# Performance work log

Measured on AMD Instinct MI355X. Metric: run time of the kernel, lower is better.

Reference implementation:

```python
import jax, jax.numpy as jnp
from jax import lax
import numpy as np

B, C, H, W, D = 4, 128, 32, 32, 32
NH = 4                 # num_heads (4*NH == 16 fc input channels)
DH = C // NH           # head dim = 32
N = H * W * D          # input_size = 32768
PROJ = 64              # proj_size
EPS = 1e-12


def setup_inputs() -> dict:
    key = jax.random.key(0)
    ks = jax.random.split(key, 12)
    s = 0.02
    return {
        "x": jax.random.normal(ks[0], (B, C, H, W, D), jnp.float32),
        "Wqkvv": jax.random.normal(ks[1], (4 * C, C), jnp.float32) * s,   # qkv_bias=False
        "W_fc": jax.random.normal(ks[2], (16, 4 * NH), jnp.float32) * s,  # Conv2d 1x1
        "b_fc": jnp.zeros((16,), jnp.float32),
        "W_dep": jax.random.normal(ks[3], (C, 16, 3, 3, 3), jnp.float32) * 0.05,  # groups=DH -> in/grp=16
        "b_dep": jnp.zeros((C,), jnp.float32),
        "W_E": jax.random.normal(ks[4], (PROJ, N), jnp.float32) * s,  # E = F (shared weights)
        "b_E": jnp.zeros((PROJ,), jnp.float32),
        "temperature": jnp.ones((NH, 1, 1), jnp.float32),
        "temperature2": jnp.ones((NH, 1, 1), jnp.float32),
        "rate": jnp.full((1,), 0.5, jnp.float32),
        "rate2": jnp.full((1,), 0.5, jnp.float32),
        "W_out": jax.random.normal(ks[5], (C // 2, C), jnp.float32) * s,
        "b_out": jnp.zeros((C // 2,), jnp.float32),
        "W_out2": jax.random.normal(ks[6], (C // 2, C), jnp.float32) * s,
        "b_out2": jnp.zeros((C // 2,), jnp.float32),
    }


def _l2norm(t):
    return t / jnp.maximum(jnp.linalg.norm(t, axis=-1, keepdims=True), EPS)


def reference(x, Wqkvv, W_fc, b_fc, W_dep, b_dep, W_E, b_E,
              temperature, temperature2, rate, rate2,
              W_out, b_out, W_out2, b_out2):
    Bc, Cc, Hc, Wc, Dc = x.shape
    Nc = Hc * Wc * Dc
    # tokens: [B, N, C]
    xf = jnp.transpose(x, (0, 2, 3, 4, 1)).reshape(Bc, Nc, Cc)
    qkvv = xf @ Wqkvv.T  # [B, N, 4C]

    # ---- fused grouped-conv branch ----
    f_all = jnp.transpose(qkvv.reshape(Bc, Nc, 4 * NH, DH), (0, 2, 1, 3))  # [B,16,N,DH]
    f = jnp.einsum('oi,bind->bond', W_fc, f_all) + b_fc[None, :, None, None]  # 1x1 conv
    f_conv = jnp.transpose(f, (0, 3, 1, 2)).reshape(Bc, 16 * DH, Hc, Wc, Dc)
    out_conv = lax.conv_general_dilated(
        f_conv, W_dep, window_strides=(1, 1, 1), padding='SAME',
        dimension_numbers=('NCDHW', 'OIDHW', 'NCDHW'), feature_group_count=DH)
    out_conv = out_conv + b_dep[None, :, None, None, None]
    out_conv = jnp.transpose(out_conv, (0, 2, 3, 4, 1)).reshape(Bc, Nc, Cc)

    # ---- dual attention ----
    qkvv5 = jnp.transpose(qkvv.reshape(Bc, Nc, 4, NH, DH), (2, 0, 3, 1, 4))  # [4,B,nh,N,dh]
    q = jnp.swapaxes(qkvv5[0], -2, -1)    # [B,nh,dh,N]
    k = jnp.swapaxes(qkvv5[1], -2, -1)
    v_CA = jnp.swapaxes(qkvv5[2], -2, -1)
    v_SA = jnp.swapaxes(qkvv5[3], -2, -1)

    k_proj = k @ W_E.T + b_E              # [B,nh,dh,proj]  (E)
    v_SA_proj = v_SA @ W_E.T + b_E        # shared weights   (F)

    qn = _l2norm(q)
    kn = _l2norm(k)

    # channel attention: [B,nh,dh,dh]
    attn_CA = jax.nn.softmax(jnp.einsum('bhdn,bhen->bhde', qn, kn) * temperature, axis=-1)
    x_CA = jnp.transpose(attn_CA @ v_CA, (0, 3, 1, 2)).reshape(Bc, Nc, Cc)  # [B,N,C]

    # spatial (Linformer-style) attention: [B,nh,N,proj]
    attn_SA = jax.nn.softmax(
        jnp.einsum('bhdn,bhdp->bhnp', qn, k_proj) * temperature2, axis=-1)
    x_SA = jnp.einsum('bhnp,bhdp->bhnd', attn_SA, v_SA_proj)  # [B,nh,N,dh]
    x_SA = jnp.transpose(x_SA, (0, 3, 1, 2)).reshape(Bc, Nc, Cc)  # faithful to torch permute

    x_SA = x_SA @ W_out.T + b_out    # [B,N,C/2]
    x_CA = x_CA @ W_out2.T + b_out2  # [B,N,C/2]
    x_attn = jnp.concatenate([x_SA, x_CA], axis=-1)
    return rate * x_attn + rate2 * out_conv
```

## Files before the change

### kernel.cpp

```cpp
#include <hip/hip_runtime.h>
#include <hip/hip_bf16.h>

typedef unsigned short u16;
typedef __attribute__((ext_vector_type(8))) short bf16x8;
typedef __attribute__((ext_vector_type(4))) float f32x4;

#define MFMA16(a,b,c) __builtin_amdgcn_mfma_f32_16x16x32_bf16((a),(b),(c),0,0,0)

__device__ __forceinline__ float bf2f(u16 u){ union{unsigned int i; float f;} v; v.i=((unsigned int)u)<<16; return v.f; }
__device__ __forceinline__ u16 f2bf(float f){ union{float f; unsigned int i;} v; v.f=f; unsigned int r=v.i+0x7fffu+((v.i>>16)&1u); return (u16)(r>>16); }
__device__ __forceinline__ unsigned int pk2(float a, float b){
  __hip_bfloat162 h = __float22bfloat162_rn(make_float2(a,b));
  union{ __hip_bfloat162 h; unsigned int u; } v; v.h = h; return v.u;
}

__global__ __launch_bounds__(256) void kcvt3(const float* __restrict__ WE, u16* __restrict__ WEb,
                                             const float* __restrict__ Wq, u16* __restrict__ Wqb,
                                             const float* __restrict__ Wo, u16* __restrict__ Wob){
  int bid = blockIdx.x;
  const float* src; u16* dst; int base;
  if(bid < 2048){ src = WE; dst = WEb; base = bid*1024; }
  else if(bid < 2112){ src = Wq; dst = Wqb; base = (bid-2048)*1024; }
  else { src = Wo; dst = Wob; base = (bid-2112)*1024; }
  int i = base + threadIdx.x*4;
  float4 v = *(const float4*)(src + i);
  ushort4 o; o.x = f2bf(v.x); o.y = f2bf(v.y); o.z = f2bf(v.z); o.w = f2bf(v.w);
  *(ushort4*)(dst + i) = o;
}

#define K1PAD 136
__global__ __launch_bounds__(256) void k1_qkvv(const float* __restrict__ x, const u16* __restrict__ Wqb, u16* __restrict__ qkvvT){
  __shared__ u16 lB[128*K1PAD];
  const int tile = blockIdx.x;
  const int b  = tile >> 8;
  const int n0 = (tile & 255) << 7;
  const int tid = threadIdx.x;
  const float* xb = x + (size_t)b*128*32768;
  {
    const int cb = (tid >> 4) << 1;
    const int m  = tid & 15;
    const int t8 = m << 3;
    const int swz = (m & 3) << 3;
    unsigned int* basep = (unsigned int*)lB;
    #pragma unroll
    for(int r=0;r<4;++r){
      const int c = cb + (r<<5);
      const float4* p0 = (const float4*)(xb + (size_t)c*32768 + n0 + t8);
      const float4* p1 = (const float4*)(xb + (size_t)(c+1)*32768 + n0 + t8);
      float4 a0 = p0[0], a1 = p0[1];
      float4 b0 = p1[0], b1 = p1[1];
      const int rot = (swz + c) & 127;
      int di = t8*68 + (rot>>1);
      basep[di      ] = pk2(a0.x, b0.x);
      basep[di+  68 ] = pk2(a0.y, b0.y);
      basep[di+ 136 ] = pk2(a0.z, b0.z);
      basep[di+ 204 ] = pk2(a0.w, b0.w);
      basep[di+ 272 ] = pk2(a1.x, b1.x);
      basep[di+ 340 ] = pk2(a1.y, b1.y);
      basep[di+ 408 ] = pk2(a1.z, b1.z);
      basep[di+ 476 ] = pk2(a1.w, b1.w);
    }
  }
  __syncthreads();
  const int wave = tid >> 6, lane = tid & 63;
  const int wm = (wave & 1) << 6;
  const int wn = (wave >> 1) << 6;
  const int lm = lane & 15, lq = lane >> 4;
  u16* outb = qkvvT + (size_t)b*512*32768;
  for(int s=0;s<4;++s){
    const int oc0 = s << 7;
    f32x4 acc[4][4] = {};
    const u16* Arow = Wqb + (oc0 + wm + lm)*128 + lq*8;
    #pragma unroll
    for(int ks=0; ks<4; ++ks){
      bf16x8 af[4], bfr[4];
      #pragma unroll
      for(int mt=0;mt<4;++mt) af[mt] = *(const bf16x8*)(Arow + mt*2048 + ks*32);
      #pragma unroll
      for(int nt=0;nt<4;++nt){
        const int tr = wn + nt*16 + lm;
        const int rot = ((((tr>>3)&3)<<3) + ks*32 + lq*8) & 127;
        bfr[nt] = *(const bf16x8*)(&lB[tr*K1PAD + rot]);
      }
      #pragma unroll
      for(int mt=0;mt<4;++mt)
        #pragma unroll
        for(int nt=0;nt<4;++nt)
          acc[mt][nt] = MFMA16(af[mt], bfr[nt], acc[mt][nt]);
    }
    #pragma unroll
    for(int mt=0;mt<4;++mt){
      const int ocr = oc0 + wm + mt*16 + lq*4;
      #pragma unroll
      for(int nt=0;nt<4;++nt){
        const int n = n0 + wn + nt*16 + lm;
        #pragma unroll
        for(int r=0;r<4;++r) outb[(size_t)(ocr+r)*32768 + n] = f2bf(acc[mt][nt][r]);
      }
    }
  }
}

__global__ void k2_weff(const float* __restrict__ Wdep, const float* __restrict__ Wfc,
                        const float* __restrict__ bdep, const float* __restrict__ bfc,
                        float* __restrict__ W_eff, float* __restrict__ bias_eff){
  int idx = blockIdx.x*256 + threadIdx.x;
  if(idx < 55296){
    int ol = idx & 3;
    int k  = (idx >> 2) % 27;
    int j  = (idx / 108) & 15;
    int g  = idx / 1728;
    int oc = g*4 + ol;
    float s = 0.f;
    for(int o=0;o<16;++o) s += Wdep[(oc*16 + o)*27 + k] * Wfc[o*16 + j];
    W_eff[idx] = s;
  }
  if(idx < 128){
    float s = bdep[idx];
    for(int o=0;o<16;++o){
      float wsum = 0.f;
      for(int k=0;k<27;++k) wsum += Wdep[(idx*16 + o)*27 + k];
      s += wsum * bfc[o];
    }
    bias_eff[idx] = s;
  }
}

__global__ __launch_bounds__(256) void k2b_norms(const u16* __restrict__ qkvvT, float* __restrict__ invn){
  const int b = blockIdx.x >> 8, c = blockIdx.x & 255;
  const u16* row = qkvvT + ((size_t)b*512 + c)*32768;
  float s = 0.f;
  for(int n = threadIdx.x*8; n < 32768; n += 2048){
    bf16x8 v = *(const bf16x8*)(row + n);
    #pragma unroll
    for(int j=0;j<8;++j){ float f = bf2f((u16)v[j]); s += f*f; }
  }
  for(int off=32; off; off>>=1) s += __shfl_down(s, off, 64);
  __shared__ float wsum[4];
  if((threadIdx.x & 63)==0) wsum[threadIdx.x>>6] = s;
  __syncthreads();
  if(threadIdx.x==0){
    float t = wsum[0]+wsum[1]+wsum[2]+wsum[3];
    invn[blockIdx.x] = 1.0f / fmaxf(sqrtf(t), 1e-12f);
  }
}

__global__ __launch_bounds__(256) void k3_proj(const u16* __restrict__ qkvvT, const u16* __restrict__ WEb,
                                               float* __restrict__ kp, float* __restrict__ vp){
  const int kc = blockIdx.x;
  const int b  = blockIdx.y;
  const int ts = blockIdx.z >> 1;
  const int rh = (blockIdx.z & 1) << 6;
  const int wave = threadIdx.x >> 6, lane = threadIdx.x & 63;
  const int lm = lane & 15, lq = lane >> 4;
  const int coff = ts ? 384 : 128;
  const u16* Arow = qkvvT + ((size_t)b*512 + coff + rh + wave*16 + lm)*32768 + kc*1024 + lq*8;
  f32x4 acc[4] = {};
  for(int ks=0; ks<32; ++ks){
    bf16x8 af = *(const bf16x8*)(Arow + ks*32);
    #pragma unroll
    for(int nt=0;nt<4;++nt){
      bf16x8 bfr = *(const bf16x8*)(WEb + (size_t)(nt*16 + lm)*32768 + kc*1024 + ks*32 + lq*8);
      acc[nt] = MFMA16(af, bfr, acc[nt]);
    }
  }
  float* out = (ts ? vp : kp) + (size_t)b*128*64;
  const int r0 = rh + wave*16 + lq*4;
  #pragma unroll
  for(int nt=0;nt<4;++nt){
    const int p = nt*16 + lm;
    #pragma unroll
    for(int r=0;r<4;++r) atomicAdd(&out[(r0+r)*64 + p], acc[nt][r]);
  }
}

__global__ __launch_bounds__(64) void k4_gram(const u16* __restrict__ qkvvT, float* __restrict__ G){
  const int kc = blockIdx.x, b = blockIdx.y, h = blockIdx.z;
  const int lane = threadIdx.x, lm = lane & 15, lq = lane >> 4;
  const u16* qb = qkvvT + ((size_t)b*512 + h*32)*32768 + kc*512 + lq*8;
  const u16* kb = qb + (size_t)128*32768;
  f32x4 acc[2][2] = {};
  for(int ks=0; ks<16; ++ks){
    bf16x8 af[2], bfr[2];
    af[0]  = *(const bf16x8*)(qb + (size_t)lm*32768 + ks*32);
    af[1]  = *(const bf16x8*)(qb + (size_t)(16+lm)*32768 + ks*32);
    bfr[0] = *(const bf16x8*)(kb + (size_t)lm*32768 + ks*32);
    bfr[1] = *(const bf16x8*)(kb + (size_t)(16+lm)*32768 + ks*32);
    #pragma unroll
    for(int mt=0;mt<2;++mt)
      #pragma unroll
      for(int nt=0;nt<2;++nt) acc[mt][nt] = MFMA16(af[mt], bfr[nt], acc[mt][nt]);
  }
  float* Gb = G + (size_t)(b*4 + h)*1024;
  #pragma unroll
  for(int mt=0;mt<2;++mt)
    #pragma unroll
    for(int nt=0;nt<2;++nt)
      #pragma unroll
      for(int r=0;r<4;++r){
        int d = mt*16 + lq*4 + r, e = nt*16 + lm;
        atomicAdd(&Gb[d*32 + e], acc[mt][nt][r]);
      }
}

__global__ __launch_bounds__(256) void k4b_softmax_m2(const float* __restrict__ G, const float* __restrict__ invn,
                                                      const float* __restrict__ temp, const float* __restrict__ Wout2,
                                                      u16* __restrict__ M2){
  const int b = blockIdx.x >> 2, h = blockIdx.x & 3;
  __shared__ float A[32][33];
  const float* Gb = G + (size_t)(b*4 + h)*1024;
  const float* inb = invn + b*256;
  const float th = temp[h];
  const int tid = threadIdx.x;
  if(tid < 32){
    const int d = tid;
    const float iq = inb[h*32 + d];
    float row[32]; float mx = -1e30f;
    #pragma unroll
    for(int e=0;e<32;++e){
      float v = Gb[d*32+e] * iq * inb[128 + h*32 + e] * th;
      row[e] = v; mx = fmaxf(mx, v);
    }
    float s = 0.f;
    #pragma unroll
    for(int e=0;e<32;++e){ float ee = __expf(row[e]-mx); row[e] = ee; s += ee; }
    const float rs = 1.0f/s;
    #pragma unroll
    for(int e=0;e<32;++e) A[d][e] = row[e]*rs;
  }
  __syncthreads();
  for(int o = tid; o < 2048; o += 256){
    const int j = o >> 5, e = o & 31;
    float s = 0.f;
    #pragma unroll
    for(int d=0;d<32;++d) s += Wout2[j*128 + h*32 + d] * A[d][e];
    M2[((size_t)b*64 + j)*128 + h*32 + e] = f2bf(s);
  }
}

__global__ __launch_bounds__(256) void k5_xsa(const u16* __restrict__ qkvvT, const float* __restrict__ kp,
                                              const float* __restrict__ vp, const float* __restrict__ invn,
                                              const float* __restrict__ bE, const float* __restrict__ temp2,
                                              u16* __restrict__ xsa){
  __shared__ __align__(16) u16 L[14336];
  __shared__ float liqt[32];
  u16* lkAh = L;
  u16* lkAl = L + 2560;
  u16* lvAh = L + 5120;
  u16* lvAl = L + 7424;
  u16* Pl   = L + 9728;
  const int b = blockIdx.z, h = blockIdx.y;
  const int tid = threadIdx.x;
  const float t2 = temp2[h];
  {
    const int p = tid >> 2, d8 = (tid & 3) << 3;
    const float be = bE[p];
    const float* kpb = kp + ((size_t)b*128 + h*32)*64;
    #pragma unroll
    for(int j=0;j<8;++j){
      float v = kpb[(size_t)(d8+j)*64 + p] + be;
      u16 hi = f2bf(v);
      lkAh[p*40 + d8 + j] = hi;
      lkAl[p*40 + d8 + j] = f2bf(v - bf2f(hi));
    }
  }
  {
    const int d = tid >> 3, p8 = (tid & 7) << 3;
    const float* vpb = vp + ((size_t)b*128 + h*32)*64;
    #pragma unroll
    for(int j=0;j<8;++j){
      float v = vpb[(size_t)d*64 + p8 + j] + bE[p8+j];
      u16 hi = f2bf(v);
      lvAh[d*72 + p8 + j] = hi;
      lvAl[d*72 + p8 + j] = f2bf(v - bf2f(hi));
    }
  }
  if(tid < 32) liqt[tid] = invn[b*256 + h*32 + tid] * t2;
  __syncthreads();
  const int wave = tid >> 6, lane = tid & 63;
  const int lm = lane & 15, lq = lane >> 4;
  const int tokw = blockIdx.x*256 + wave*64;
  const u16* qb = qkvvT + ((size_t)b*512 + h*32)*32768;
  float iq[8];
  #pragma unroll
  for(int j=0;j<8;++j) iq[j] = liqt[lq*8+j];
  u16* PW = Pl + wave*1152 + lm*72;
  u16* ob = xsa + (((size_t)b*4 + h)*32)*32768;
  for(int nt=0; nt<4; ++nt){
    const int tok = tokw + nt*16 + lm;
    union { u16 u[8]; bf16x8 v; } qh, ql;
    #pragma unroll
    for(int j=0;j<8;++j){
      float qv = bf2f(qb[(size_t)(lq*8+j)*32768 + tok]) * iq[j];
      u16 hi = f2bf(qv);
      qh.u[j] = hi;
      ql.u[j] = f2bf(qv - bf2f(hi));
    }
    f32x4 accS[4];
    #pragma unroll
    for(int mt=0;mt<4;++mt){
      bf16x8 Ah = *(const bf16x8*)(lkAh + (mt*16+lm)*40 + lq*8);
      bf16x8 Al = *(const bf16x8*)(lkAl + (mt*16+lm)*40 + lq*8);
      f32x4 a = {};
      a = MFMA16(Ah, qh.v, a);
      a = MFMA16(Ah, ql.v, a);
      a = MFMA16(Al, qh.v, a);
      accS[mt] = a;
    }
    float mx = -1e30f;
    #pragma unroll
    for(int mt=0;mt<4;++mt)
      mx = fmaxf(mx, fmaxf(fmaxf(accS[mt][0],accS[mt][1]), fmaxf(accS[mt][2],accS[mt][3])));
    mx = fmaxf(mx, __shfl_xor(mx,16));
    mx = fmaxf(mx, __shfl_xor(mx,32));
    float pexp[4][4];
    float sum = 0.f;
    #pragma unroll
    for(int mt=0;mt<4;++mt)
      #pragma unroll
      for(int r=0;r<4;++r){ float e = __expf(accS[mt][r]-mx); pexp[mt][r]=e; sum+=e; }
    sum += __shfl_xor(sum,16);
    sum += __shfl_xor(sum,32);
    const float rinv = 1.0f/sum;
    #pragma unroll
    for(int mt=0;mt<4;++mt){
      *(unsigned int*)(PW + mt*16 + lq*4)     = pk2(pexp[mt][0], pexp[mt][1]);
      *(unsigned int*)(PW + mt*16 + lq*4 + 2) = pk2(pexp[mt][2], pexp[mt][3]);
    }
    f32x4 accO[2] = {};
    #pragma unroll
    for(int ks=0;ks<2;++ks){
      bf16x8 Pb = *(const bf16x8*)(PW + ks*32 + lq*8);
      #pragma unroll
      for(int mt=0;mt<2;++mt){
        bf16x8 Avh = *(const bf16x8*)(lvAh + (mt*16+lm)*72 + ks*32 + lq*8);
        bf16x8 Avl = *(const bf16x8*)(lvAl + (mt*16+lm)*72 + ks*32 + lq*8);
        accO[mt] = MFMA16(Avh, Pb, accO[mt]);
        accO[mt] = MFMA16(Avl, Pb, accO[mt]);
      }
    }
    #pragma unroll
    for(int mt=0;mt<2;++mt)
      #pragma unroll
      for(int r=0;r<4;++r)
        ob[(size_t)(mt*16+lq*4+r)*32768 + tok] = f2bf(accO[mt][r]*rinv);
  }
}

#define CSX 36
#define CSZ 360
__global__ __launch_bounds__(256,6) void kconv(const u16* __restrict__ qkvvT, const float* __restrict__ W_eff,
                                               const float* __restrict__ bias_eff, u16* __restrict__ convo){
  __shared__ float lf[10*CSZ];
  const int zt = blockIdx.x >> 2, yt = blockIdx.x & 3;
  const int g = blockIdx.y, b = blockIdx.z;
  const int tid = threadIdx.x;
  const int z0 = zt << 3, y0 = yt << 3;
  const int lz = tid >> 5;
  const int vy = (tid >> 2) & 7;
  const int x0 = (tid & 3) << 3;
  float acc[4][8];
  #pragma unroll
  for(int oc=0;oc<4;++oc)
    #pragma unroll
    for(int xi=0;xi<8;++xi) acc[oc][xi] = 0.f;
  const u16* qb = qkvvT + (size_t)b*512*32768;
  const int sz = tid / 10, sy = tid - sz*10;
  const int gz = z0 + sz - 1, gy = y0 + sy - 1;
  const bool srow_ok = (tid < 100) && ((unsigned)gz < 32u) && ((unsigned)gy < 32u);
  float2* d2 = (float2*)&lf[sz*CSZ + sy*CSX];
  const float* Wgbase = W_eff + (size_t)(g*16)*108;

  for(int p=0;p<16;++p){
    __syncthreads();
    if(tid < 100){
      if(srow_ok){
        const u16* src = qb + ((size_t)(p*32 + g))*32768 + gz*1024 + gy*32;
        float carry = 0.f;
        #pragma unroll
        for(int q=0;q<4;++q){
          bf16x8 v = *(const bf16x8*)(src + q*8);
          float w0=bf2f((u16)v[0]), w1=bf2f((u16)v[1]), w2=bf2f((u16)v[2]), w3=bf2f((u16)v[3]);
          float w4=bf2f((u16)v[4]), w5=bf2f((u16)v[5]), w6=bf2f((u16)v[6]), w7=bf2f((u16)v[7]);
          d2[q*4+0] = make_float2(carry, w0);
          d2[q*4+1] = make_float2(w1, w2);
          d2[q*4+2] = make_float2(w3, w4);
          d2[q*4+3] = make_float2(w5, w6);
          carry = w7;
        }
        d2[16] = make_float2(carry, 0.f);
      } else {
        #pragma unroll
        for(int i=0;i<17;++i) d2[i] = make_float2(0.f, 0.f);
      }
    }
    __syncthreads();
    const float* Wg = Wgbase + p*108;
    #pragma unroll
    for(int dy=0;dy<3;++dy){
      #pragma unroll
      for(int dz=0;dz<3;++dz){
        const float* row = &lf[(lz+dz)*CSZ + (vy+dy)*CSX + x0];
        float4 fa = *(const float4*)(row);
        float4 fb = *(const float4*)(row+4);
        float2 fc = *(const float2*)(row+8);
        float fw[10] = {fa.x,fa.y,fa.z,fa.w, fb.x,fb.y,fb.z,fb.w, fc.x,fc.y};
        const float* Wb = Wg + (dz*3+dy)*12;
        #pragma unroll
        for(int kx=0;kx<3;++kx){
          float4 wv = *(const float4*)(Wb + kx*4);
          #pragma unroll
          for(int xi=0;xi<8;++xi){
            float f = fw[xi+kx];
            acc[0][xi] += wv.x*f; acc[1][xi] += wv.y*f;
            acc[2][xi] += wv.z*f; acc[3][xi] += wv.w*f;
          }
        }
      }
    }
  }
  const float4 bi = *(const float4*)(bias_eff + g*4);
  const int nb = (z0 + lz)*1024 + (y0+vy)*32 + x0;
  u16* ob = convo + ((size_t)b*32768 + nb)*128 + g*4;
  #pragma unroll
  for(int xi=0;xi<8;++xi){
    unsigned long long pk = (unsigned long long)f2bf(acc[0][xi] + bi.x)
                          | ((unsigned long long)f2bf(acc[1][xi] + bi.y) << 16)
                          | ((unsigned long long)f2bf(acc[2][xi] + bi.z) << 32)
                          | ((unsigned long long)f2bf(acc[3][xi] + bi.w) << 48);
    *(unsigned long long*)(ob + (size_t)xi*128) = pk;
  }
}

#define K6PAD 136
__global__ __launch_bounds__(256) void k6_out(const u16* __restrict__ qkvvT, const u16* __restrict__ xsa,
                                              const u16* __restrict__ conv, const u16* __restrict__ M2,
                                              const u16* __restrict__ Woutb, const float* __restrict__ bout,
                                              const float* __restrict__ bout2, const float* __restrict__ rate,
                                              const float* __restrict__ rate2, float* __restrict__ out){
  __shared__ u16 lA[128*K6PAD];
  const int tile = blockIdx.x;
  const int b  = tile >> 8;
  const int n0 = (tile & 255) << 7;
  const int tid = threadIdx.x;
  const int hh = (n0 >> 8) & 3;
  const int dh = n0 >> 10;
  const u16* xseg = xsa + (((size_t)b*4 + hh)*32 + dh)*32768 + ((size_t)(n0 & 255) << 7);
  {
    const int r = tid >> 1, off = (tid & 1) << 6;
    const u16* src = xseg + r*128 + off;
    u16* dst = &lA[r*K6PAD + off];
    #pragma unroll
    for(int q=0;q<8;++q) *(bf16x8*)(dst + q*8) = *(const bf16x8*)(src + q*8);
  }
  __syncthreads();
  const int wave = tid >> 6, lane = tid & 63;
  const int lm = lane & 15, lq = lane >> 4;
  f32x4 accS[2][4] = {};
  #pragma unroll
  for(int ks=0;ks<4;++ks){
    bf16x8 a0 = *(const bf16x8*)(&lA[(wave*32 + lm)*K6PAD + ks*32 + lq*8]);
    bf16x8 a1 = *(const bf16x8*)(&lA[(wave*32 + 16 + lm)*K6PAD + ks*32 + lq*8]);
    #pragma unroll
    for(int nt=0;nt<4;++nt){
      bf16x8 bw = *(const bf16x8*)(Woutb + (nt*16 + lm)*128 + ks*32 + lq*8);
      accS[0][nt] = MFMA16(a0, bw, accS[0][nt]);
      accS[1][nt] = MFMA16(a1, bw, accS[1][nt]);
    }
  }
  __syncthreads();
  {
    const int cb = tid >> 4, t8 = (tid & 15) << 3;
    const u16* vb = qkvvT + ((size_t)b*512 + 256)*32768 + n0;
    #pragma unroll
    for(int r2=0;r2<8;++r2){
      int c = cb + (r2<<4);
      bf16x8 v = *(const bf16x8*)(vb + (size_t)c*32768 + t8);
      #pragma unroll
      for(int j=0;j<8;++j) lA[(t8+j)*K6PAD + c] = (u16)v[j];
    }
  }
  __syncthreads();
  f32x4 accC[2][4] = {};
  #pragma unroll
  for(int ks=0;ks<4;++ks){
    bf16x8 a0 = *(const bf16x8*)(&lA[(wave*32 + lm)*K6PAD + ks*32 + lq*8]);
    bf16x8 a1 = *(const bf16x8*)(&lA[(wave*32 + 16 + lm)*K6PAD + ks*32 + lq*8]);
    #pragma unroll
    for(int nt=0;nt<4;++nt){
      bf16x8 bm = *(const bf16x8*)(M2 + ((size_t)b*64 + nt*16 + lm)*128 + ks*32 + lq*8);
      accC[0][nt] = MFMA16(a0, bm, accC[0][nt]);
      accC[1][nt] = MFMA16(a1, bm, accC[1][nt]);
    }
  }
  const float rt = rate[0], rt2 = rate2[0];
  float* ob = out + ((size_t)b*32768 + n0)*128;
  const u16* cbp = conv + ((size_t)b*32768 + n0)*128;
  #pragma unroll
  for(int mt=0;mt<2;++mt){
    #pragma unroll
    for(int r=0;r<4;++r){
      const int tok = wave*32 + mt*16 + lq*4 + r;
      #pragma unroll
      for(int nt=0;nt<4;++nt){
        const int j = nt*16 + lm;
        float sa = accS[mt][nt][r] + bout[j];
        float ca = accC[mt][nt][r] + bout2[j];
        float c1 = bf2f(cbp[(size_t)tok*128 + j]);
        float c2 = bf2f(cbp[(size_t)tok*128 + 64 + j]);
        ob[(size_t)tok*128 + j]      = rt*sa + rt2*c1;
        ob[(size_t)tok*128 + 64 + j] = rt*ca + rt2*c2;
      }
    }
  }
}

extern "C" void kernel_launch(void* const* d_in, const int* in_sizes, int n_in,
                              void* d_out, int out_size, void* d_ws, size_t ws_size,
                              hipStream_t stream){
  const float* x     = (const float*)d_in[0];
  const float* Wq    = (const float*)d_in[1];
  const float* Wfc   = (const float*)d_in[2];
  const float* bfc   = (const float*)d_in[3];
  const float* Wdep  = (const float*)d_in[4];
  const float* bdep  = (const float*)d_in[5];
  const float* WE    = (const float*)d_in[6];
  const float* bE    = (const float*)d_in[7];
  const float* temp  = (const float*)d_in[8];
  const float* temp2 = (const float*)d_in[9];
  const float* rate  = (const float*)d_in[10];
  const float* rate2 = (const float*)d_in[11];
  const float* Wout  = (const float*)d_in[12];
  const float* bout  = (const float*)d_in[13];
  const float* Wout2 = (const float*)d_in[14];
  const float* bout2 = (const float*)d_in[15];
  float* outp = (float*)d_out;

  char* w = (char*)d_ws;
  size_t off = 0;
  auto alloc = [&](size_t bytes)->char*{ char* p = w + off; off += (bytes + 255) & ~(size_t)255; return p; };
  u16*   qkvvT  = (u16*)  alloc((size_t)4*512*32768*2);
  u16*   xsa    = (u16*)  alloc((size_t)4*4*32*32768*2);
  u16*   convb  = (u16*)  alloc((size_t)4*32768*128*2);
  float* W_eff  = (float*)alloc(55296*4);
  float* biasef = (float*)alloc(128*4);
  float* invn   = (float*)alloc(1024*4);
  float* kp     = (float*)alloc(32768*4);
  float* vp     = (float*)alloc(32768*4);
  float* G      = (float*)alloc(16384*4);
  u16*   M2     = (u16*)  alloc(32768*2);
  u16*   WEb    = (u16*)  alloc((size_t)2097152*2);
  u16*   Wqb    = (u16*)  alloc(65536*2);
  u16*   Woutb  = (u16*)  alloc(8192*2);

  hipMemsetAsync(kp, 0, (size_t)(32768+32768+16384)*4, stream);

  kcvt3         <<<2120,          256, 0, stream>>>(WE, WEb, Wq, Wqb, Wout, Woutb);
  k1_qkvv       <<<1024,          256, 0, stream>>>(x, Wqb, qkvvT);
  k2_weff       <<<216,           256, 0, stream>>>(Wdep, Wfc, bdep, bfc, W_eff, biasef);
  k2b_norms     <<<1024,          256, 0, stream>>>(qkvvT, invn);
  k3_proj       <<<dim3(32,4,4),  256, 0, stream>>>(qkvvT, WEb, kp, vp);
  k4_gram       <<<dim3(64,4,4),   64, 0, stream>>>(qkvvT, G);
  k4b_softmax_m2<<<16,            256, 0, stream>>>(G, invn, temp, Wout2, M2);
  k5_xsa        <<<dim3(128,4,4), 256, 0, stream>>>(qkvvT, kp, vp, invn, bE, temp2, xsa);
  kconv         <<<dim3(16,32,4), 256, 0, stream>>>(qkvvT, W_eff, biasef, convb);
  k6_out        <<<1024,          256, 0, stream>>>(qkvvT, xsa, convb, M2, Woutb, bout, bout2, rate, rate2, outp);
}
```

Before: 556.3 us.

## Fuse conv, projection, gram and norm kernels into one interleaved launch

Merges the depthwise conv, the k/v Linformer projection, the q·k gram reduction and the row L2 norms into a single kernel. The kernel dispatches work by block index, interleaving 8 conv blocks with 7 reduction blocks in each group of 15. This lets the compute-bound conv overlap with the memory-bound reductions and removes three launches and the tail gaps between them. In exchange, all branches share the conv's register and LDS footprint and its occupancy bound, and the gram work is regrouped to four waves per block.

Result: faster. 540.8 us (-2.8%).

```diff
diff --git a/kernel.cpp b/kernel.cpp
--- a/kernel.cpp
+++ b/kernel.cpp
@@ -126,81 +126,177 @@
   }
 }
 
-__global__ __launch_bounds__(256) void k2b_norms(const u16* __restrict__ qkvvT, float* __restrict__ invn){
-  const int b = blockIdx.x >> 8, c = blockIdx.x & 255;
-  const u16* row = qkvvT + ((size_t)b*512 + c)*32768;
-  float s = 0.f;
-  for(int n = threadIdx.x*8; n < 32768; n += 2048){
-    bf16x8 v = *(const bf16x8*)(row + n);
-    #pragma unroll
-    for(int j=0;j<8;++j){ float f = bf2f((u16)v[j]); s += f*f; }
-  }
-  for(int off=32; off; off>>=1) s += __shfl_down(s, off, 64);
+#define CSX 36
+#define CSZ 360
+__global__ __launch_bounds__(256,6) void kmega(const u16* __restrict__ qkvvT, const float* __restrict__ W_eff,
+                                               const float* __restrict__ bias_eff, u16* __restrict__ convo,
+                                               const u16* __restrict__ WEb, float* __restrict__ kp,
+                                               float* __restrict__ vp, float* __restrict__ G,
+                                               float* __restrict__ invn){
+  __shared__ float lf[10*CSZ];
   __shared__ float wsum[4];
-  if((threadIdx.x & 63)==0) wsum[threadIdx.x>>6] = s;
-  __syncthreads();
-  if(threadIdx.x==0){
-    float t = wsum[0]+wsum[1]+wsum[2]+wsum[3];
-    invn[blockIdx.x] = 1.0f / fmaxf(sqrtf(t), 1e-12f);
-  }
-}
-
-__global__ __launch_bounds__(256) void k3_proj(const u16* __restrict__ qkvvT, const u16* __restrict__ WEb,
-                                               float* __restrict__ kp, float* __restrict__ vp){
-  const int kc = blockIdx.x;
-  const int b  = blockIdx.y;
-  const int ts = blockIdx.z >> 1;
-  const int rh = (blockIdx.z & 1) << 6;
-  const int wave = threadIdx.x >> 6, lane = threadIdx.x & 63;
-  const int lm = lane & 15, lq = lane >> 4;
-  const int coff = ts ? 384 : 128;
-  const u16* Arow = qkvvT + ((size_t)b*512 + coff + rh + wave*16 + lm)*32768 + kc*1024 + lq*8;
-  f32x4 acc[4] = {};
-  for(int ks=0; ks<32; ++ks){
-    bf16x8 af = *(const bf16x8*)(Arow + ks*32);
+  const int bid = blockIdx.x;
+  const int gq = bid / 15, rr = bid - gq*15;
+  const int tid = threadIdx.x;
+
+  if(rr < 8){
+    const int cidx = gq*8 + rr;
+    const int gx = cidx & 15, g = (cidx>>4)&31, b = cidx>>9;
+    const int zt = gx >> 2, yt = gx & 3;
+    const int z0 = zt << 3, y0 = yt << 3;
+    const int lz = tid >> 5;
+    const int vy = (tid >> 2) & 7;
+    const int x0 = (tid & 3) << 3;
+    float acc[4][8];
+    #pragma unroll
+    for(int oc=0;oc<4;++oc)
+      #pragma unroll
+      for(int xi=0;xi<8;++xi) acc[oc][xi] = 0.f;
+    const u16* qb = qkvvT + (size_t)b*512*32768;
+    const int sz = tid / 10, sy = tid - sz*10;
+    const int gz = z0 + sz - 1, gy = y0 + sy - 1;
+    const bool srow_ok = (tid < 100) && ((unsigned)gz < 32u) && ((unsigned)gy < 32u);
+    float2* d2 = (float2*)&lf[sz*CSZ + sy*CSX];
+    const float* Wgbase = W_eff + (size_t)(g*16)*108;
+
+    for(int p=0;p<16;++p){
+      __syncthreads();
+      if(tid < 100){
+        if(srow_ok){
+          const u16* src = qb + ((size_t)(p*32 + g))*32768 + gz*1024 + gy*32;
+          float carry = 0.f;
+          #pragma unroll
+          for(int q=0;q<4;++q){
+            bf16x8 v = *(const bf16x8*)(src + q*8);
+            float w0=bf2f((u16)v[0]), w1=bf2f((u16)v[1]), w2=bf2f((u16)v[2]), w3=bf2f((u16)v[3]);
+            float w4=bf2f((u16)v[4]), w5=bf2f((u16)v[5]), w6=bf2f((u16)v[6]), w7=bf2f((u16)v[7]);
+            d2[q*4+0] = make_float2(carry, w0);
+            d2[q*4+1] = make_float2(w1, w2);
+            d2[q*4+2] = make_float2(w3, w4);
+            d2[q*4+3] = make_float2(w5, w6);
+            carry = w7;
+          }
+          d2[16] = make_float2(carry, 0.f);
+        } else {
+          #pragma unroll
+          for(int i=0;i<17;++i) d2[i] = make_float2(0.f, 0.f);
+        }
+      }
+      __syncthreads();
+      const float* Wg = Wgbase + p*108;
+      #pragma unroll
+      for(int dy=0;dy<3;++dy){
+        #pragma unroll
+        for(int dz=0;dz<3;++dz){
+          const float* row = &lf[(lz+dz)*CSZ + (vy+dy)*CSX + x0];
+          float4 fa = *(const float4*)(row);
+          float4 fb = *(const float4*)(row+4);
+          float2 fc = *(const float2*)(row+8);
+          float fw[10] = {fa.x,fa.y,fa.z,fa.w, fb.x,fb.y,fb.z,fb.w, fc.x,fc.y};
+          const float* Wb = Wg + (dz*3+dy)*12;
+          #pragma unroll
+          for(int kx=0;kx<3;++kx){
+            float4 wv = *(const float4*)(Wb + kx*4);
+            #pragma unroll
+            for(int xi=0;xi<8;++xi){
+              float f = fw[xi+kx];
+              acc[0][xi] += wv.x*f; acc[1][xi] += wv.y*f;
+              acc[2][xi] += wv.z*f; acc[3][xi] += wv.w*f;
+            }
+          }
+        }
+      }
+    }
+    const float4 bi = *(const float4*)(bias_eff + g*4);
+    const int nb = (z0 + lz)*1024 + (y0+vy)*32 + x0;
+    u16* ob = convo + ((size_t)b*32768 + nb)*128 + g*4;
+    #pragma unroll
+    for(int xi=0;xi<8;++xi){
+      unsigned long long pk = (unsigned long long)f2bf(acc[0][xi] + bi.x)
+                            | ((unsigned long long)f2bf(acc[1][xi] + bi.y) << 16)
+                            | ((unsigned long long)f2bf(acc[2][xi] + bi.z) << 32)
+                            | ((unsigned long long)f2bf(acc[3][xi] + bi.w) << 48);
+      *(unsigned long long*)(ob + (size_t)xi*128) = pk;
+    }
+    return;
+  }
+
+  const int oidx = gq*7 + (rr - 8);
+  if(oidx < 512){
+    const int kc = oidx & 31;
+    const int b  = (oidx >> 5) & 3;
+    const int zz = oidx >> 7;
+    const int ts = zz >> 1;
+    const int rh = (zz & 1) << 6;
+    const int wave = tid >> 6, lane = tid & 63;
+    const int lm = lane & 15, lq = lane >> 4;
+    const int coff = ts ? 384 : 128;
+    const u16* Arow = qkvvT + ((size_t)b*512 + coff + rh + wave*16 + lm)*32768 + kc*1024 + lq*8;
+    f32x4 acc[4] = {};
+    for(int ks=0; ks<32; ++ks){
+      bf16x8 af = *(const bf16x8*)(Arow + ks*32);
+      #pragma unroll
+      for(int nt=0;nt<4;++nt){
+        bf16x8 bfr = *(const bf16x8*)(WEb + (size_t)(nt*16 + lm)*32768 + kc*1024 + ks*32 + lq*8);
+        acc[nt] = MFMA16(af, bfr, acc[nt]);
+      }
+    }
+    float* out = (ts ? vp : kp) + (size_t)b*128*64;
+    const int r0 = rh + wave*16 + lq*4;
     #pragma unroll
     for(int nt=0;nt<4;++nt){
-      bf16x8 bfr = *(const bf16x8*)(WEb + (size_t)(nt*16 + lm)*32768 + kc*1024 + ks*32 + lq*8);
-      acc[nt] = MFMA16(af, bfr, acc[nt]);
-    }
-  }
-  float* out = (ts ? vp : kp) + (size_t)b*128*64;
-  const int r0 = rh + wave*16 + lq*4;
-  #pragma unroll
-  for(int nt=0;nt<4;++nt){
-    const int p = nt*16 + lm;
-    #pragma unroll
-    for(int r=0;r<4;++r) atomicAdd(&out[(r0+r)*64 + p], acc[nt][r]);
-  }
-}
-
-__global__ __launch_bounds__(64) void k4_gram(const u16* __restrict__ qkvvT, float* __restrict__ G){
-  const int kc = blockIdx.x, b = blockIdx.y, h = blockIdx.z;
-  const int lane = threadIdx.x, lm = lane & 15, lq = lane >> 4;
-  const u16* qb = qkvvT + ((size_t)b*512 + h*32)*32768 + kc*512 + lq*8;
-  const u16* kb = qb + (size_t)128*32768;
-  f32x4 acc[2][2] = {};
-  for(int ks=0; ks<16; ++ks){
-    bf16x8 af[2], bfr[2];
-    af[0]  = *(const bf16x8*)(qb + (size_t)lm*32768 + ks*32);
-    af[1]  = *(const bf16x8*)(qb + (size_t)(16+lm)*32768 + ks*32);
-    bfr[0] = *(const bf16x8*)(kb + (size_t)lm*32768 + ks*32);
-    bfr[1] = *(const bf16x8*)(kb + (size_t)(16+lm)*32768 + ks*32);
+      const int p = nt*16 + lm;
+      #pragma unroll
+      for(int r=0;r<4;++r) atomicAdd(&out[(r0+r)*64 + p], acc[nt][r]);
+    }
+  } else if(oidx < 768){
+    const int idx2 = oidx - 512;
+    const int h = idx2 & 3, b = (idx2>>2)&3, kcg = idx2 >> 4;
+    const int wave = tid >> 6, lane = tid & 63;
+    const int kc = kcg*4 + wave;
+    const int lm = lane & 15, lq = lane >> 4;
+    const u16* qb = qkvvT + ((size_t)b*512 + h*32)*32768 + kc*512 + lq*8;
+    const u16* kb = qb + (size_t)128*32768;
+    f32x4 acc[2][2] = {};
+    for(int ks=0; ks<16; ++ks){
+      bf16x8 af[2], bfr[2];
+      af[0]  = *(const bf16x8*)(qb + (size_t)lm*32768 + ks*32);
+      af[1]  = *(const bf16x8*)(qb + (size_t)(16+lm)*32768 + ks*32);
+      bfr[0] = *(const bf16x8*)(kb + (size_t)lm*32768 + ks*32);
+      bfr[1] = *(const bf16x8*)(kb + (size_t)(16+lm)*32768 + ks*32);
+      #pragma unroll
+      for(int mt=0;mt<2;++mt)
+        #pragma unroll
+        for(int nt=0;nt<2;++nt) acc[mt][nt] = MFMA16(af[mt], bfr[nt], acc[mt][nt]);
+    }
+    float* Gb = G + (size_t)(b*4 + h)*1024;
     #pragma unroll
     for(int mt=0;mt<2;++mt)
       #pragma unroll
-      for(int nt=0;nt<2;++nt) acc[mt][nt] = MFMA16(af[mt], bfr[nt], acc[mt][nt]);
-  }
-  float* Gb = G + (size_t)(b*4 + h)*1024;
-  #pragma unroll
-  for(int mt=0;mt<2;++mt)
-    #pragma unroll
-    for(int nt=0;nt<2;++nt)
-      #pragma unroll
-      for(int r=0;r<4;++r){
-        int d = mt*16 + lq*4 + r, e = nt*16 + lm;
-        atomicAdd(&Gb[d*32 + e], acc[mt][nt][r]);
-      }
+      for(int nt=0;nt<2;++nt)
+        #pragma unroll
+        for(int r=0;r<4;++r){
+          int d = mt*16 + lq*4 + r, e = nt*16 + lm;
+          atomicAdd(&Gb[d*32 + e], acc[mt][nt][r]);
+        }
+  } else {
+    const int idx4 = oidx - 768;
+    const int b = idx4 >> 8, c = idx4 & 255;
+    const u16* row = qkvvT + ((size_t)b*512 + c)*32768;
+    float s = 0.f;
+    for(int n = tid*8; n < 32768; n += 2048){
+      bf16x8 v = *(const bf16x8*)(row + n);
+      #pragma unroll
+      for(int j=0;j<8;++j){ float f = bf2f((u16)v[j]); s += f*f; }
+    }
+    for(int off=32; off; off>>=1) s += __shfl_down(s, off, 64);
+    if((tid & 63)==0) wsum[tid>>6] = s;
+    __syncthreads();
+    if(tid==0){
+      float t = wsum[0]+wsum[1]+wsum[2]+wsum[3];
+      invn[idx4] = 1.0f / fmaxf(sqrtf(t), 1e-12f);
+    }
+  }
 }
 
 __global__ __launch_bounds__(256) void k4b_softmax_m2(const float* __restrict__ G, const float* __restrict__ invn,
@@ -344,91 +440,6 @@
       #pragma unroll
       for(int r=0;r<4;++r)
         ob[(size_t)(mt*16+lq*4+r)*32768 + tok] = f2bf(accO[mt][r]*rinv);
-  }
-}
-
-#define CSX 36
-#define CSZ 360
-__global__ __launch_bounds__(256,6) void kconv(const u16* __restrict__ qkvvT, const float* __restrict__ W_eff,
-                                               const float* __restrict__ bias_eff, u16* __restrict__ convo){
-  __shared__ float lf[10*CSZ];
-  const int zt = blockIdx.x >> 2, yt = blockIdx.x & 3;
-  const int g = blockIdx.y, b = blockIdx.z;
-  const int tid = threadIdx.x;
-  const int z0 = zt << 3, y0 = yt << 3;
-  const int lz = tid >> 5;
-  const int vy = (tid >> 2) & 7;
-  const int x0 = (tid & 3) << 3;
-  float acc[4][8];
-  #pragma unroll
-  for(int oc=0;oc<4;++oc)
-    #pragma unroll
-    for(int xi=0;xi<8;++xi) acc[oc][xi] = 0.f;
-  const u16* qb = qkvvT + (size_t)b*512*32768;
-  const int sz = tid / 10, sy = tid - sz*10;
-  const int gz = z0 + sz - 1, gy = y0 + sy - 1;
-  const bool srow_ok = (tid < 100) && ((unsigned)gz < 32u) && ((unsigned)gy < 32u);
-  float2* d2 = (float2*)&lf[sz*CSZ + sy*CSX];
-  const float* Wgbase = W_eff + (size_t)(g*16)*108;
-
-  for(int p=0;p<16;++p){
-    __syncthreads();
-    if(tid < 100){
-      if(srow_ok){
-        const u16* src = qb + ((size_t)(p*32 + g))*32768 + gz*1024 + gy*32;
-        float carry = 0.f;
-        #pragma unroll
-        for(int q=0;q<4;++q){
-          bf16x8 v = *(const bf16x8*)(src + q*8);
-          float w0=bf2f((u16)v[0]), w1=bf2f((u16)v[1]), w2=bf2f((u16)v[2]), w3=bf2f((u16)v[3]);
-          float w4=bf2f((u16)v[4]), w5=bf2f((u16)v[5]), w6=bf2f((u16)v[6]), w7=bf2f((u16)v[7]);
-          d2[q*4+0] = make_float2(carry, w0);
-          d2[q*4+1] = make_float2(w1, w2);
-          d2[q*4+2] = make_float2(w3, w4);
-          d2[q*4+3] = make_float2(w5, w6);
-          carry = w7;
-        }
-        d2[16] = make_float2(carry, 0.f);
-      } else {
-        #pragma unroll
-        for(int i=0;i<17;++i) d2[i] = make_float2(0.f, 0.f);
-      }
-    }
-    __syncthreads();
-    const float* Wg = Wgbase + p*108;
-    #pragma unroll
-    for(int dy=0;dy<3;++dy){
-      #pragma unroll
-      for(int dz=0;dz<3;++dz){
-        const float* row = &lf[(lz+dz)*CSZ + (vy+dy)*CSX + x0];
-        float4 fa = *(const float4*)(row);
-        float4 fb = *(const float4*)(row+4);
-        float2 fc = *(const float2*)(row+8);
-        float fw[10] = {fa.x,fa.y,fa.z,fa.w, fb.x,fb.y,fb.z,fb.w, fc.x,fc.y};
-        const float* Wb = Wg + (dz*3+dy)*12;
-        #pragma unroll
-        for(int kx=0;kx<3;++kx){
-          float4 wv = *(const float4*)(Wb + kx*4);
-          #pragma unroll
-          for(int xi=0;xi<8;++xi){
-            float f = fw[xi+kx];
-            acc[0][xi] += wv.x*f; acc[1][xi] += wv.y*f;
-            acc[2][xi] += wv.z*f; acc[3][xi] += wv.w*f;
-          }
-        }
-      }
-    }
-  }
-  const float4 bi = *(const float4*)(bias_eff + g*4);
-  const int nb = (z0 + lz)*1024 + (y0+vy)*32 + x0;
-  u16* ob = convo + ((size_t)b*32768 + nb)*128 + g*4;
-  #pragma unroll
-  for(int xi=0;xi<8;++xi){
-    unsigned long long pk = (unsigned long long)f2bf(acc[0][xi] + bi.x)
-                          | ((unsigned long long)f2bf(acc[1][xi] + bi.y) << 16)
-                          | ((unsigned long long)f2bf(acc[2][xi] + bi.z) << 32)
-                          | ((unsigned long long)f2bf(acc[3][xi] + bi.w) << 48);
-    *(unsigned long long*)(ob + (size_t)xi*128) = pk;
   }
 }
 
@@ -558,11 +569,8 @@
   kcvt3         <<<2120,          256, 0, stream>>>(WE, WEb, Wq, Wqb, Wout, Woutb);
   k1_qkvv       <<<1024,          256, 0, stream>>>(x, Wqb, qkvvT);
   k2_weff       <<<216,           256, 0, stream>>>(Wdep, Wfc, bdep, bfc, W_eff, biasef);
-  k2b_norms     <<<1024,          256, 0, stream>>>(qkvvT, invn);
-  k3_proj       <<<dim3(32,4,4),  256, 0, stream>>>(qkvvT, WEb, kp, vp);
-  k4_gram       <<<dim3(64,4,4),   64, 0, stream>>>(qkvvT, G);
+  kmega         <<<3840,          256, 0, stream>>>(qkvvT, W_eff, biasef, convb, WEb, kp, vp, G, invn);
   k4b_softmax_m2<<<16,            256, 0, stream>>>(G, invn, temp, Wout2, M2);
   k5_xsa        <<<dim3(128,4,4), 256, 0, stream>>>(qkvvT, kp, vp, invn, bE, temp2, xsa);
-  kconv         <<<dim3(16,32,4), 256, 0, stream>>>(qkvvT, W_eff, biasef, convb);
   k6_out        <<<1024,          256, 0, stream>>>(qkvvT, xsa, convb, M2, Woutb, bout, bout2, rate, rate2, outp);
 }
```
